# Kernel optimization log

Hardware: AMD Instinct MI355X
Metric: run time of the kernel (lower is better)

## Reference

```python
import jax, jax.numpy as jnp
import numpy as np

# SMPL-H kintree parents for the first 22 joints (kintree_table[0][:22]); root parent is unused.
SMPL_PARENT = np.array([0, 0, 0, 0, 1, 2, 3, 4, 5, 6, 7, 8, 9, 9, 9, 12, 13, 14, 16, 17, 18, 19], dtype=np.int64)

EPS = 1e-12


def _sixd2matrot(d6):
    # d6: [..., 6] -> R: [..., 3, 3] (rows b1,b2,b3), pytorch3d rotation_6d_to_matrix convention
    a1, a2 = d6[..., :3], d6[..., 3:]
    b1 = a1 / jnp.maximum(jnp.linalg.norm(a1, axis=-1, keepdims=True), EPS)
    a2p = a2 - jnp.sum(b1 * a2, axis=-1, keepdims=True) * b1
    b2 = a2p / jnp.maximum(jnp.linalg.norm(a2p, axis=-1, keepdims=True), EPS)
    b3 = jnp.cross(b1, b2)
    return jnp.stack([b1, b2, b3], axis=-2)


def setup_inputs() -> dict:
    key = jax.random.key(0)
    B, T, J = 512, 196, 22
    pred_pose = jax.random.normal(key, (B, T, J * 6), dtype=jnp.float32)
    return {"pred_pose": pred_pose, "parent": SMPL_PARENT}


def reference(pred_pose, parent):
    B, T, C = pred_pose.shape  # C = 22*6
    J = C // 6
    parent = np.asarray(parent)  # static tree structure
    d6 = pred_pose.reshape(B * T, J, 6)
    R_local = _sixd2matrot(d6)  # [N, J, 3, 3]
    # forward kinematics along the tree: R_global[i] = R_global[parent[i]] @ R_local[i]
    R_global = [R_local[:, 0]]
    for i in range(1, J):
        R_global.append(jnp.einsum('nij,njk->nik', R_global[int(parent[i])], R_local[:, i]))
    R_global = jnp.stack(R_global, axis=1)  # [N, J, 3, 3]
    # matrot -> 6d: first two rows flattened
    rotation_global_r6d = R_global[..., :2, :].reshape(B, T, J * 6)
    return rotation_global_r6d
```

## Files before the change

### kernel.cpp

```cpp
#include <hip/hip_runtime.h>


#define TPB 512
#define TILE_FRAMES 16
#define TILE_FLOATS (TILE_FRAMES * 132)

namespace {
constexpr int PAR1[22] = {0,0,0,0,1,2,3,4,5,6,7,8,9,9,9,12,13,14,16,17,18,19};
constexpr int PAR2[22] = {0,0,0,0,0,0,0,1,2,3,4,5,6,6,6,9,9,9,13,14,16,17};
constexpr int PAR4[22] = {0,0,0,0,0,0,0,0,0,0,0,0,0,0,0,3,3,3,6,6,9,9};

__device__ __host__ constexpr unsigned long long pack5(const int (&t)[22], int base) {
    unsigned long long v = 0;
    for (int i = 0; i < 11; ++i)
        v |= (unsigned long long)(t[base + i] & 31) << (5 * i);
    return v;
}
constexpr unsigned long long P1L = pack5(PAR1, 0), P1H = pack5(PAR1, 11);
constexpr unsigned long long P2L = pack5(PAR2, 0), P2H = pack5(PAR2, 11);
constexpr unsigned long long P4L = pack5(PAR4, 0), P4H = pack5(PAR4, 11);
}

__device__ __forceinline__ void mm3(float* __restrict__ D, const float* __restrict__ P,
                                    const float* __restrict__ L) {
#pragma unroll
    for (int r = 0; r < 3; ++r)
#pragma unroll
        for (int c = 0; c < 3; ++c)
            D[3 * r + c] = P[3 * r + 0] * L[0 + c] +
                           P[3 * r + 1] * L[3 + c] +
                           P[3 * r + 2] * L[6 + c];
}

__global__ __launch_bounds__(TPB, 6) void fk6d_kernel(const float* __restrict__ in,
                                                      float* __restrict__ out)
{
    __shared__ float lds[TILE_FLOATS];
    const int tid = threadIdx.x;
    const int wid = tid >> 6;
    const int lane = tid & 63;

    const float* gin = in + (size_t)blockIdx.x * TILE_FLOATS;
    float* gout = out + (size_t)blockIdx.x * TILE_FLOATS;

    __builtin_amdgcn_global_load_lds(
        (const __attribute__((address_space(1))) void*)(gin + wid * 256 + lane * 4),
        (__attribute__((address_space(3))) void*)(lds + wid * 256), 16, 0, 0);
    if (wid == 0) {
        __builtin_amdgcn_global_load_lds(
            (const __attribute__((address_space(1))) void*)(gin + 2048 + lane),
            (__attribute__((address_space(3))) void*)(lds + 2048), 4, 0, 0);
    }
    __syncthreads();

    const int base = lane & 32;
    const int j = lane & 31;
    const int frame = wid * 2 + (lane >> 5);
    const bool act = (j < 22);
    const int jc = act ? j : 21;
    const int jm = (jc < 11) ? jc : jc - 11;
    const int sh = 5 * jm;
    const int a1 = (int)(((jc < 11) ? P1L : P1H) >> sh) & 31;
    const int a2 = (int)(((jc < 11) ? P2L : P2H) >> sh) & 31;
    const int a4 = (int)(((jc < 11) ? P4L : P4H) >> sh) & 31;

    float A[9];
#pragma unroll
    for (int k = 0; k < 9; ++k) A[k] = 0.0f;
    if (act) {
        const float* s = lds + frame * 132 + j * 6;
        float2 d0 = *reinterpret_cast<const float2*>(s);
        float2 d1 = *reinterpret_cast<const float2*>(s + 2);
        float2 d2 = *reinterpret_cast<const float2*>(s + 4);
        float a1x = d0.x, a1y = d0.y, a1z = d1.x;
        float a2x = d1.y, a2y = d2.x, a2z = d2.y;
        float n1 = sqrtf(a1x * a1x + a1y * a1y + a1z * a1z);
        float i1 = 1.0f / fmaxf(n1, 1e-12f);
        float b1x = a1x * i1, b1y = a1y * i1, b1z = a1z * i1;
        float dt = b1x * a2x + b1y * a2y + b1z * a2z;
        float cx = a2x - dt * b1x, cy = a2y - dt * b1y, cz = a2z - dt * b1z;
        float n2 = sqrtf(cx * cx + cy * cy + cz * cz);
        float i2 = 1.0f / fmaxf(n2, 1e-12f);
        A[0] = b1x; A[1] = b1y; A[2] = b1z;
        A[3] = cx * i2; A[4] = cy * i2; A[5] = cz * i2;
        A[6] = A[1] * A[5] - A[2] * A[4];
        A[7] = A[2] * A[3] - A[0] * A[5];
        A[8] = A[0] * A[4] - A[1] * A[3];
    }

    {
        float M[9], T[9];
        int src = base | a1;
#pragma unroll
        for (int k = 0; k < 9; ++k) M[k] = __shfl(A[k], src, 64);
        mm3(T, M, A);
        bool on = (j >= 1);
#pragma unroll
        for (int k = 0; k < 9; ++k) A[k] = on ? T[k] : A[k];
    }
    {
        float M[9], T[9];
        int src = base | a2;
#pragma unroll
        for (int k = 0; k < 9; ++k) M[k] = __shfl(A[k], src, 64);
        mm3(T, M, A);
        bool on = (j >= 4);
#pragma unroll
        for (int k = 0; k < 9; ++k) A[k] = on ? T[k] : A[k];
    }
    {
        float M[9], T[9];
        int src = base | a4;
#pragma unroll
        for (int k = 0; k < 9; ++k) M[k] = __shfl(A[k], src, 64);
        mm3(T, M, A);
        bool on = (j >= 10);
#pragma unroll
        for (int k = 0; k < 9; ++k) A[k] = on ? T[k] : A[k];
    }

    if (act) {
        float* d = lds + frame * 132 + j * 6;
        *reinterpret_cast<float2*>(d)     = make_float2(A[0], A[1]);
        *reinterpret_cast<float2*>(d + 2) = make_float2(A[2], A[3]);
        *reinterpret_cast<float2*>(d + 4) = make_float2(A[4], A[5]);
    }
    __syncthreads();

    const float4* l4 = reinterpret_cast<const float4*>(lds);
    float4* o4 = reinterpret_cast<float4*>(gout);
#pragma unroll
    for (int t = tid; t < TILE_FLOATS / 4; t += TPB) o4[t] = l4[t];
}

__global__ void fk6d_tail(const float* __restrict__ in, float* __restrict__ out,
                          int n0, int N) {
    constexpr int PAR[22] = {0, 0, 0, 0, 1, 2, 3, 4, 5, 6, 7, 8, 9, 9, 9,
                             12, 13, 14, 16, 17, 18, 19};
    int n = n0 + blockIdx.x * blockDim.x + threadIdx.x;
    if (n >= N) return;
    const float* src = in + (size_t)n * 132;
    float* dst = out + (size_t)n * 132;
    float Rg[22][9];
#pragma unroll
    for (int j = 0; j < 22; ++j) {
        const float* s = src + 6 * j;
        float Lr[9];
        float n1 = sqrtf(s[0]*s[0] + s[1]*s[1] + s[2]*s[2]);
        float i1 = 1.0f / fmaxf(n1, 1e-12f);
        float b1x = s[0]*i1, b1y = s[1]*i1, b1z = s[2]*i1;
        float dt = b1x*s[3] + b1y*s[4] + b1z*s[5];
        float cx = s[3]-dt*b1x, cy = s[4]-dt*b1y, cz = s[5]-dt*b1z;
        float n2 = sqrtf(cx*cx + cy*cy + cz*cz);
        float i2 = 1.0f / fmaxf(n2, 1e-12f);
        Lr[0]=b1x; Lr[1]=b1y; Lr[2]=b1z;
        Lr[3]=cx*i2; Lr[4]=cy*i2; Lr[5]=cz*i2;
        Lr[6]=Lr[1]*Lr[5]-Lr[2]*Lr[4];
        Lr[7]=Lr[2]*Lr[3]-Lr[0]*Lr[5];
        Lr[8]=Lr[0]*Lr[4]-Lr[1]*Lr[3];
        if (j == 0) {
#pragma unroll
            for (int k = 0; k < 9; ++k) Rg[0][k] = Lr[k];
        } else {
            mm3(Rg[j], Rg[PAR[j]], Lr);
        }
#pragma unroll
        for (int k = 0; k < 6; ++k) dst[6 * j + k] = Rg[j][k];
    }
}

extern "C" void kernel_launch(void* const* d_in, const int* in_sizes, int n_in,
                              void* d_out, int out_size, void* d_ws, size_t ws_size,
                              hipStream_t stream) {
    const float* in = (const float*)d_in[0];
    float* out = (float*)d_out;
    int N = in_sizes[0] / 132;
    int NT = N / TILE_FRAMES;
    if (NT > 0) fk6d_kernel<<<NT, TPB, 0, stream>>>(in, out);
    int rem = N - NT * TILE_FRAMES;
    if (rem > 0)
        fk6d_tail<<<(rem + 63) / 64, 64, 0, stream>>>(in, out, NT * TILE_FRAMES, N);
}
```

Measured before the change: 29.79 us.

## Process each 16-frame tile with a single wavefront looping over frame pairs

Shrinks the block from 512 threads to one 64-lane wavefront. That wavefront loads the whole 16-frame tile to LDS, loops over 8 frame pairs doing the shuffle-based FK, and writes the tile back. The goal is to cut the cost of block-wide barriers and to amortise per-block setup such as the parent-index decode across more work per lane. In exchange, each block now runs its frames serially, and occupancy depends on how many 8.4KB-LDS single-wave blocks fit per CU. The last global_load_lds also changes from 4-byte to 16-byte loads.

```diff
diff --git a/kernel.cpp b/kernel.cpp
--- a/kernel.cpp
+++ b/kernel.cpp
@@ -1,7 +1,7 @@
 #include <hip/hip_runtime.h>
 
 
-#define TPB 512
+#define TPB 64
 #define TILE_FRAMES 16
 #define TILE_FLOATS (TILE_FRAMES * 132)
 
@@ -32,105 +32,104 @@
                            P[3 * r + 2] * L[6 + c];
 }
 
-__global__ __launch_bounds__(TPB, 6) void fk6d_kernel(const float* __restrict__ in,
+__global__ __launch_bounds__(TPB, 4) void fk6d_kernel(const float* __restrict__ in,
                                                       float* __restrict__ out)
 {
     __shared__ float lds[TILE_FLOATS];
-    const int tid = threadIdx.x;
-    const int wid = tid >> 6;
-    const int lane = tid & 63;
+    const int lane = threadIdx.x;
+    const int col = lane >> 5;
+    const int base = lane & 32;
+    const int j = lane & 31;
 
     const float* gin = in + (size_t)blockIdx.x * TILE_FLOATS;
     float* gout = out + (size_t)blockIdx.x * TILE_FLOATS;
 
-    __builtin_amdgcn_global_load_lds(
-        (const __attribute__((address_space(1))) void*)(gin + wid * 256 + lane * 4),
-        (__attribute__((address_space(3))) void*)(lds + wid * 256), 16, 0, 0);
-    if (wid == 0) {
+#pragma unroll
+    for (int k = 0; k < 8; ++k)
         __builtin_amdgcn_global_load_lds(
-            (const __attribute__((address_space(1))) void*)(gin + 2048 + lane),
-            (__attribute__((address_space(3))) void*)(lds + 2048), 4, 0, 0);
-    }
+            (const __attribute__((address_space(1))) void*)(gin + k * 256 + lane * 4),
+            (__attribute__((address_space(3))) void*)(lds + k * 256), 16, 0, 0);
+    if (lane < 16)
+        __builtin_amdgcn_global_load_lds(
+            (const __attribute__((address_space(1))) void*)(gin + 2048 + lane * 4),
+            (__attribute__((address_space(3))) void*)(lds + 2048), 16, 0, 0);
     __syncthreads();
 
-    const int base = lane & 32;
-    const int j = lane & 31;
-    const int frame = wid * 2 + (lane >> 5);
     const bool act = (j < 22);
     const int jc = act ? j : 21;
     const int jm = (jc < 11) ? jc : jc - 11;
     const int sh = 5 * jm;
-    const int a1 = (int)(((jc < 11) ? P1L : P1H) >> sh) & 31;
-    const int a2 = (int)(((jc < 11) ? P2L : P2H) >> sh) & 31;
-    const int a4 = (int)(((jc < 11) ? P4L : P4H) >> sh) & 31;
+    const int s1 = base | ((int)(((jc < 11) ? P1L : P1H) >> sh) & 31);
+    const int s2 = base | ((int)(((jc < 11) ? P2L : P2H) >> sh) & 31);
+    const int s4 = base | ((int)(((jc < 11) ? P4L : P4H) >> sh) & 31);
+    const bool on1 = (j >= 1), on2 = (j >= 4), on3 = (j >= 10);
 
-    float A[9];
+#pragma unroll 2
+    for (int fp = 0; fp < 8; ++fp) {
+        const int frame = 2 * fp + col;
+        float* slot = lds + frame * 132 + j * 6;
+
+        float A[9];
 #pragma unroll
-    for (int k = 0; k < 9; ++k) A[k] = 0.0f;
-    if (act) {
-        const float* s = lds + frame * 132 + j * 6;
-        float2 d0 = *reinterpret_cast<const float2*>(s);
-        float2 d1 = *reinterpret_cast<const float2*>(s + 2);
-        float2 d2 = *reinterpret_cast<const float2*>(s + 4);
-        float a1x = d0.x, a1y = d0.y, a1z = d1.x;
-        float a2x = d1.y, a2y = d2.x, a2z = d2.y;
-        float n1 = sqrtf(a1x * a1x + a1y * a1y + a1z * a1z);
-        float i1 = 1.0f / fmaxf(n1, 1e-12f);
-        float b1x = a1x * i1, b1y = a1y * i1, b1z = a1z * i1;
-        float dt = b1x * a2x + b1y * a2y + b1z * a2z;
-        float cx = a2x - dt * b1x, cy = a2y - dt * b1y, cz = a2z - dt * b1z;
-        float n2 = sqrtf(cx * cx + cy * cy + cz * cz);
-        float i2 = 1.0f / fmaxf(n2, 1e-12f);
-        A[0] = b1x; A[1] = b1y; A[2] = b1z;
-        A[3] = cx * i2; A[4] = cy * i2; A[5] = cz * i2;
-        A[6] = A[1] * A[5] - A[2] * A[4];
-        A[7] = A[2] * A[3] - A[0] * A[5];
-        A[8] = A[0] * A[4] - A[1] * A[3];
-    }
+        for (int k = 0; k < 9; ++k) A[k] = 0.0f;
+        if (act) {
+            float2 d0 = *reinterpret_cast<const float2*>(slot);
+            float2 d1 = *reinterpret_cast<const float2*>(slot + 2);
+            float2 d2 = *reinterpret_cast<const float2*>(slot + 4);
+            float a1x = d0.x, a1y = d0.y, a1z = d1.x;
+            float a2x = d1.y, a2y = d2.x, a2z = d2.y;
+            float n1 = sqrtf(a1x * a1x + a1y * a1y + a1z * a1z);
+            float i1 = 1.0f / fmaxf(n1, 1e-12f);
+            float b1x = a1x * i1, b1y = a1y * i1, b1z = a1z * i1;
+            float dt = b1x * a2x + b1y * a2y + b1z * a2z;
+            float cx = a2x - dt * b1x, cy = a2y - dt * b1y, cz = a2z - dt * b1z;
+            float n2 = sqrtf(cx * cx + cy * cy + cz * cz);
+            float i2 = 1.0f / fmaxf(n2, 1e-12f);
+            A[0] = b1x; A[1] = b1y; A[2] = b1z;
+            A[3] = cx * i2; A[4] = cy * i2; A[5] = cz * i2;
+            A[6] = A[1] * A[5] - A[2] * A[4];
+            A[7] = A[2] * A[3] - A[0] * A[5];
+            A[8] = A[0] * A[4] - A[1] * A[3];
+        }
 
-    {
-        float M[9], T[9];
-        int src = base | a1;
+        {
+            float M[9], T[9];
 #pragma unroll
-        for (int k = 0; k < 9; ++k) M[k] = __shfl(A[k], src, 64);
-        mm3(T, M, A);
-        bool on = (j >= 1);
+            for (int k = 0; k < 9; ++k) M[k] = __shfl(A[k], s1, 64);
+            mm3(T, M, A);
 #pragma unroll
-        for (int k = 0; k < 9; ++k) A[k] = on ? T[k] : A[k];
-    }
-    {
-        float M[9], T[9];
-        int src = base | a2;
+            for (int k = 0; k < 9; ++k) A[k] = on1 ? T[k] : A[k];
+        }
+        {
+            float M[9], T[9];
 #pragma unroll
-        for (int k = 0; k < 9; ++k) M[k] = __shfl(A[k], src, 64);
-        mm3(T, M, A);
-        bool on = (j >= 4);
+            for (int k = 0; k < 9; ++k) M[k] = __shfl(A[k], s2, 64);
+            mm3(T, M, A);
 #pragma unroll
-        for (int k = 0; k < 9; ++k) A[k] = on ? T[k] : A[k];
-    }
-    {
-        float M[9], T[9];
-        int src = base | a4;
+            for (int k = 0; k < 9; ++k) A[k] = on2 ? T[k] : A[k];
+        }
+        {
+            float M[9], T[9];
 #pragma unroll
-        for (int k = 0; k < 9; ++k) M[k] = __shfl(A[k], src, 64);
-        mm3(T, M, A);
-        bool on = (j >= 10);
+            for (int k = 0; k < 9; ++k) M[k] = __shfl(A[k], s4, 64);
+            mm3(T, M, A);
 #pragma unroll
-        for (int k = 0; k < 9; ++k) A[k] = on ? T[k] : A[k];
-    }
+            for (int k = 0; k < 9; ++k) A[k] = on3 ? T[k] : A[k];
+        }
 
-    if (act) {
-        float* d = lds + frame * 132 + j * 6;
-        *reinterpret_cast<float2*>(d)     = make_float2(A[0], A[1]);
-        *reinterpret_cast<float2*>(d + 2) = make_float2(A[2], A[3]);
-        *reinterpret_cast<float2*>(d + 4) = make_float2(A[4], A[5]);
+        if (act) {
+            *reinterpret_cast<float2*>(slot)     = make_float2(A[0], A[1]);
+            *reinterpret_cast<float2*>(slot + 2) = make_float2(A[2], A[3]);
+            *reinterpret_cast<float2*>(slot + 4) = make_float2(A[4], A[5]);
+        }
     }
     __syncthreads();
 
     const float4* l4 = reinterpret_cast<const float4*>(lds);
     float4* o4 = reinterpret_cast<float4*>(gout);
 #pragma unroll
-    for (int t = tid; t < TILE_FLOATS / 4; t += TPB) o4[t] = l4[t];
+    for (int k = 0; k < 8; ++k) o4[k * 64 + lane] = l4[k * 64 + lane];
+    if (lane < 16) o4[512 + lane] = l4[512 + lane];
 }
 
 __global__ void fk6d_tail(const float* __restrict__ in, float* __restrict__ out,
@@ -143,8 +142,8 @@
     float* dst = out + (size_t)n * 132;
     float Rg[22][9];
 #pragma unroll
-    for (int j = 0; j < 22; ++j) {
-        const float* s = src + 6 * j;
+    for (int jj = 0; jj < 22; ++jj) {
+        const float* s = src + 6 * jj;
         float Lr[9];
         float n1 = sqrtf(s[0]*s[0] + s[1]*s[1] + s[2]*s[2]);
         float i1 = 1.0f / fmaxf(n1, 1e-12f);
@@ -158,14 +157,14 @@
         Lr[6]=Lr[1]*Lr[5]-Lr[2]*Lr[4];
         Lr[7]=Lr[2]*Lr[3]-Lr[0]*Lr[5];
         Lr[8]=Lr[0]*Lr[4]-Lr[1]*Lr[3];
-        if (j == 0) {
+        if (jj == 0) {
 #pragma unroll
             for (int k = 0; k < 9; ++k) Rg[0][k] = Lr[k];
         } else {
-            mm3(Rg[j], Rg[PAR[j]], Lr);
+            mm3(Rg[jj], Rg[PAR[jj]], Lr);
         }
 #pragma unroll
-        for (int k = 0; k < 6; ++k) dst[6 * j + k] = Rg[j][k];
+        for (int k = 0; k < 6; ++k) dst[6 * jj + k] = Rg[jj][k];
     }
 }
 
```

Result: slower. 32.77 us (+10.0%).
